# Optimization experiments

Measured on AMD Instinct MI355X. Metric: run time of the kernel, lower is better.

## Reference

```python
import jax, jax.numpy as jnp
import numpy as np

B, V, N, IN_F, HEADS, OUT_F = 4, 4, 1000, 64, 4, 32
D = HEADS * OUT_F  # 128, concat=True
E = 64000
NEG_SLOPE = 0.2


def setup_inputs() -> dict:
    key = jax.random.key(0)
    ks = jax.random.split(key, 8)
    x = jax.random.normal(ks[0], (B, V, N, IN_F), jnp.float32)
    edge_index = jax.random.randint(ks[1], (2, E), 0, B * N, dtype=jnp.int64)
    W = jax.random.normal(ks[2], (HEADS * OUT_F, IN_F), jnp.float32) / np.sqrt(IN_F)
    att = jax.random.normal(ks[3], (1, HEADS, 2 * OUT_F), jnp.float32) * 0.1
    in_proj_w = jax.random.normal(ks[4], (3 * D, D), jnp.float32) / np.sqrt(D)
    in_proj_b = jnp.zeros((3 * D,), jnp.float32)
    out_proj_w = jax.random.normal(ks[5], (D, D), jnp.float32) / np.sqrt(D)
    out_proj_b = jnp.zeros((D,), jnp.float32)
    bias = jnp.zeros((D,), jnp.float32)
    return dict(x=x, W=W, att=att, in_proj_w=in_proj_w, in_proj_b=in_proj_b,
                out_proj_w=out_proj_w, out_proj_b=out_proj_b, bias=bias,
                edge_index=edge_index)


def reference(x, W, att, in_proj_w, in_proj_b, out_proj_w, out_proj_b, bias, edge_index):
    Bx, Vx, Nx, _ = x.shape
    Ntot = Bx * Nx
    # intra-view GAT: shared W across views
    h = jnp.einsum('bvni,oi->bvno', x, W).reshape(Bx, Vx, Nx, HEADS, OUT_F)
    # block-diagonal placement: h_full[b*V+v, b*N:(b+1)*N] = h[b,v]
    ib = jnp.arange(Bx)
    hf = jnp.zeros((Bx, Vx, Bx, Nx, HEADS, OUT_F), x.dtype).at[ib, :, ib].set(h)
    h_full = hf.reshape(Bx * Vx, Ntot, HEADS, OUT_F)
    # add self loops
    loops = jnp.arange(Ntot, dtype=edge_index.dtype)
    src = jnp.concatenate([edge_index[0], loops])
    dst = jnp.concatenate([edge_index[1], loops])
    # attention scores (faithful to source: flatten h_full over (B*V, Ntot) and
    # index with raw node ids, i.e. gathers from block 0 only)
    h_flat = h_full.reshape(Bx * Vx * Ntot, HEADS, OUT_F)
    h_cat = jnp.concatenate([h_flat[src], h_flat[dst]], axis=-1)  # [Etot, H, 2*OUT]
    att_in = jax.nn.leaky_relu(h_cat, NEG_SLOPE)
    scores = jnp.sum(att * att_in, axis=-1)  # [Etot, HEADS]
    # per-destination segment softmax
    seg_max = jax.ops.segment_max(scores, dst, num_segments=Ntot)
    seg_max = jax.lax.stop_gradient(jnp.where(jnp.isfinite(seg_max), seg_max, 0.0))
    ex = jnp.exp(scores - seg_max[dst])
    denom = jax.ops.segment_sum(ex, dst, num_segments=Ntot)
    alpha = ex / (denom[dst] + 1e-16)  # [Etot, HEADS]
    # scatter-add aggregation, broadcast over B*V rows
    msgs = h_full[:, src] * alpha[None, :, :, None]  # [B*V, Etot, H, OUT]
    out_full = jnp.zeros_like(h_full).at[:, dst].add(msgs)
    # extract each graph's own node block
    out = out_full.reshape(Bx, Vx, Bx, Nx, HEADS, OUT_F)[ib, :, ib]  # [B,V,N,H,OUT]
    h_gat = out.reshape(Bx, Vx, Nx, HEADS * OUT_F)  # concat heads
    # inter-view mixing: MHA over the V axis per node
    seq = h_gat.transpose(0, 2, 1, 3).reshape(Bx * Nx, Vx, D)
    q, k, v = jnp.split(seq @ in_proj_w.T + in_proj_b, 3, axis=-1)
    hd = D // HEADS
    sp = lambda t: t.reshape(Bx * Nx, Vx, HEADS, hd).transpose(0, 2, 1, 3)
    q, k, v = sp(q), sp(k), sp(v)
    aw = jax.nn.softmax(jnp.einsum('bhqd,bhkd->bhqk', q, k) / jnp.sqrt(jnp.asarray(hd, x.dtype)), axis=-1)
    ao = jnp.einsum('bhqk,bhkd->bhqd', aw, v).transpose(0, 2, 1, 3).reshape(Bx * Nx, Vx, D)
    mixed = ao @ out_proj_w.T + out_proj_b
    h_mixed = mixed.reshape(Bx, Nx, Vx, D).transpose(0, 2, 1, 3)  # [B,V,N,D]
    return h_mixed + bias
```

## Files before the change

kernel.cpp:

```cpp
#include <hip/hip_runtime.h>

#define NN 1000
#define HEADS_ 4
#define DM 128
#define EE 64000
#define NTOT 4000
#define ETOT 68000
#define CAP 48

template <int K, int SCORE, int REMAP>
__global__ __launch_bounds__(256) void gemm_kernel(const float* __restrict__ A,
                                                   const float* __restrict__ Wt,
                                                   const float* __restrict__ b1,
                                                   const float* __restrict__ b2,
                                                   float* __restrict__ C, int N,
                                                   const float* __restrict__ att,
                                                   float* __restrict__ ssrc,
                                                   float* __restrict__ sdst) {
  __shared__ float As[128 * 64];
  __shared__ float Bs[64 * 64];
  int tid = threadIdx.x;
  int m0 = blockIdx.x * 128, n0 = blockIdx.y * 64;
  int tx = tid & 15, ty = tid >> 4;
  const float4* A4 = (const float4*)A;
  const float4* W4 = (const float4*)Wt;
  float acc[8][4] = {};

  for (int c = 0; c < K / 64; ++c) {
    __syncthreads();
    {
      int q = tid & 15;
      int r0 = tid >> 4;
#pragma unroll
      for (int p = 0; p < 8; ++p) {
        int r = r0 + p * 16;
        float4 v = A4[(size_t)(m0 + r) * (K / 4) + c * 16 + q];
        *(float4*)&As[r * 64 + ((q ^ (r & 15)) << 2)] = v;
      }
#pragma unroll
      for (int p = 0; p < 4; ++p) {
        int r = r0 + p * 16;
        float4 v = W4[(size_t)(n0 + r) * (K / 4) + c * 16 + q];
        *(float4*)&Bs[r * 64 + ((q ^ (r & 15)) << 2)] = v;
      }
    }
    __syncthreads();
#pragma unroll 4
    for (int q = 0; q < 16; ++q) {
      float4 a[8], b[4];
#pragma unroll
      for (int i = 0; i < 8; ++i) {
        int r = ty * 8 + i;
        a[i] = *(const float4*)&As[r * 64 + ((q ^ (r & 15)) << 2)];
      }
#pragma unroll
      for (int j = 0; j < 4; ++j) {
        int rn = tx * 4 + j;
        b[j] = *(const float4*)&Bs[rn * 64 + ((q ^ (rn & 15)) << 2)];
      }
#pragma unroll
      for (int i = 0; i < 8; ++i)
#pragma unroll
        for (int j = 0; j < 4; ++j)
          acc[i][j] += a[i].x * b[j].x + a[i].y * b[j].y
                     + a[i].z * b[j].z + a[i].w * b[j].w;
    }
  }

  float bd[4] = {0.f, 0.f, 0.f, 0.f};
  int nc = n0 + tx * 4;
  if (b1) { bd[0] = b1[nc]; bd[1] = b1[nc+1]; bd[2] = b1[nc+2]; bd[3] = b1[nc+3]; }
  if (b2) { bd[0] += b2[nc]; bd[1] += b2[nc+1]; bd[2] += b2[nc+2]; bd[3] += b2[nc+3]; }
#pragma unroll
  for (int i = 0; i < 8; ++i) {
    int m = m0 + ty * 8 + i;
    int om = m;
    if (REMAP) {
      int node = m >> 2, v = m & 3;
      int b = node / NN, n = node - b * NN;
      om = (b * 4 + v) * NN + n;
    }
    float4 o = make_float4(acc[i][0] + bd[0], acc[i][1] + bd[1],
                           acc[i][2] + bd[2], acc[i][3] + bd[3]);
    *(float4*)&C[(size_t)om * N + nc] = o;
  }

  if (SCORE && m0 < NN) {
    int hsel = tx >> 3;
    int h = (int)blockIdx.y * 2 + hsel;
    int kb = (tx & 7) * 4;
    float a0[4], a1[4];
#pragma unroll
    for (int j = 0; j < 4; ++j) {
      a0[j] = att[h * 64 + kb + j];
      a1[j] = att[h * 64 + 32 + kb + j];
    }
#pragma unroll
    for (int i = 0; i < 8; ++i) {
      int m = m0 + ty * 8 + i;
      float p0 = 0.f, p1 = 0.f;
#pragma unroll
      for (int j = 0; j < 4; ++j) {
        float g = acc[i][j];
        float lr = g > 0.f ? g : 0.2f * g;
        p0 += a0[j] * lr;
        p1 += a1[j] * lr;
      }
      p0 += __shfl_xor(p0, 1, 16); p1 += __shfl_xor(p1, 1, 16);
      p0 += __shfl_xor(p0, 2, 16); p1 += __shfl_xor(p1, 2, 16);
      p0 += __shfl_xor(p0, 4, 16); p1 += __shfl_xor(p1, 4, 16);
      if ((tx & 7) == 0 && m < NN) {
        ssrc[m * HEADS_ + h] = p0;
        sdst[m * HEADS_ + h] = p1;
      }
    }
  }
}

__global__ void edge_score_kernel(const int* __restrict__ ei,
                                  const float* __restrict__ ssrc,
                                  const float* __restrict__ sdst,
                                  float* __restrict__ exbuf,
                                  float* __restrict__ denom,
                                  int* __restrict__ cnt,
                                  int2* __restrict__ elist) {
  int e = blockIdx.x * blockDim.x + threadIdx.x;
  if (e >= ETOT) return;
  int s, d;
  if (e < EE) { s = ei[e]; d = ei[EE + e]; }
  else { s = d = e - EE; }
#pragma unroll
  for (int h = 0; h < HEADS_; ++h) {
    float sc = ssrc[s * HEADS_ + h] + sdst[d * HEADS_ + h];
    float ex = __expf(sc);
    exbuf[e * HEADS_ + h] = ex;
    atomicAdd(&denom[d * HEADS_ + h], ex);
  }
  if (s / NN == d / NN) {
    int pos = atomicAdd(&cnt[d], 1);
    if (pos < CAP) elist[d * CAP + pos] = make_int2(s, e);
  }
}

__global__ __launch_bounds__(256) void gather_kernel(const int* __restrict__ cnt,
                                                     const int2* __restrict__ elist,
                                                     const float* __restrict__ exbuf,
                                                     const float* __restrict__ denom,
                                                     const float* __restrict__ hbuf,
                                                     float* __restrict__ hgat) {
  int li = threadIdx.x >> 7;
  int t = threadIdx.x & 127;
  int d = blockIdx.x * 2 + li;
  int v = t >> 5, q = t & 31;
  int h = q >> 3;
  int b = d / NN;
  float rd = 1.f / (denom[d * HEADS_ + h] + 1e-16f);
  float4 acc = make_float4(0.f, 0.f, 0.f, 0.f);
  int m = cnt[d]; if (m > CAP) m = CAP;
  const int2* el = elist + d * CAP;
  const float* hbase = hbuf + ((size_t)(b * 4 + v) * NN) * DM + q * 4;
  for (int i = 0; i < m; ++i) {
    int2 se = el[i];
    float alpha = exbuf[se.y * HEADS_ + h] * rd;
    int sl = se.x - b * NN;
    float4 hv = *(const float4*)(hbase + (size_t)sl * DM);
    acc.x += alpha * hv.x; acc.y += alpha * hv.y;
    acc.z += alpha * hv.z; acc.w += alpha * hv.w;
  }
  *(float4*)&hgat[((size_t)(d * 4 + v)) * DM + q * 4] = acc;
}

__global__ __launch_bounds__(256) void attn_kernel(const float* __restrict__ qkv,
                                                   float* __restrict__ ao) {
  int li = threadIdx.x >> 7;
  int t = threadIdx.x & 127;
  int node = blockIdx.x * 2 + li;
  __shared__ float qs[2][4][DM], ks[2][4][DM], vs[2][4][DM];
  __shared__ float aw[2][4][HEADS_][4];
#pragma unroll
  for (int v = 0; v < 4; ++v) {
    size_t base = (size_t)(node * 4 + v) * 384;
    qs[li][v][t] = qkv[base + t];
    ks[li][v][t] = qkv[base + 128 + t];
    vs[li][v][t] = qkv[base + 256 + t];
  }
  __syncthreads();
  if (t < 64) {
    int vq = t >> 4, vk = (t >> 2) & 3, h = t & 3;
    float acc = 0.f;
#pragma unroll
    for (int kd = 0; kd < 32; ++kd)
      acc += qs[li][vq][h * 32 + kd] * ks[li][vk][h * 32 + kd];
    aw[li][vq][h][vk] = acc * 0.17677669529663687f;
  }
  __syncthreads();
  if (t < 16) {
    int vq = t >> 2, h = t & 3;
    float m = aw[li][vq][h][0];
    for (int i = 1; i < 4; ++i) m = fmaxf(m, aw[li][vq][h][i]);
    float e[4], s = 0.f;
    for (int i = 0; i < 4; ++i) { e[i] = __expf(aw[li][vq][h][i] - m); s += e[i]; }
    for (int i = 0; i < 4; ++i) aw[li][vq][h][i] = e[i] / s;
  }
  __syncthreads();
  int h = t >> 5;
#pragma unroll
  for (int vq = 0; vq < 4; ++vq) {
    float acc = 0.f;
#pragma unroll
    for (int vk = 0; vk < 4; ++vk) acc += aw[li][vq][h][vk] * vs[li][vk][t];
    ao[(size_t)(node * 4 + vq) * DM + t] = acc;
  }
}

extern "C" void kernel_launch(void* const* d_in, const int* in_sizes, int n_in,
                              void* d_out, int out_size, void* d_ws, size_t ws_size,
                              hipStream_t stream) {
  const float* x    = (const float*)d_in[0];
  const float* W    = (const float*)d_in[1];
  const float* att  = (const float*)d_in[2];
  const float* inw  = (const float*)d_in[3];
  const float* inb  = (const float*)d_in[4];
  const float* outw = (const float*)d_in[5];
  const float* outb = (const float*)d_in[6];
  const float* bias = (const float*)d_in[7];
  const int*   ei   = (const int*)d_in[8];
  float* out = (float*)d_out;

  float* ws = (float*)d_ws;
  float* hbuf  = ws;
  float* hgat  = ws + 2100000;
  float* qkv   = ws + 4200000;
  float* ao    = ws + 10400000;
  float* ssrc  = ws + 12500000;
  float* sdst  = ssrc + 16000;
  float* denom = sdst + 16000;
  int*   cnt   = (int*)(denom + 16000);
  float* exbuf = (float*)(cnt + 4000);
  int2*  elist = (int2*)(exbuf + 272000);

  hipMemsetAsync(ssrc, 0, 52000 * sizeof(float), stream);

  gemm_kernel<64, 1, 0><<<dim3(125, 2), 256, 0, stream>>>(
      x, W, nullptr, nullptr, hbuf, 128, att, ssrc, sdst);
  edge_score_kernel<<<(ETOT + 255) / 256, 256, 0, stream>>>(
      ei, ssrc, sdst, exbuf, denom, cnt, elist);
  gather_kernel<<<NTOT / 2, 256, 0, stream>>>(cnt, elist, exbuf, denom, hbuf, hgat);
  gemm_kernel<128, 0, 0><<<dim3(125, 6), 256, 0, stream>>>(
      hgat, inw, inb, nullptr, qkv, 384, nullptr, nullptr, nullptr);
  attn_kernel<<<NTOT / 2, 256, 0, stream>>>(qkv, ao);
  gemm_kernel<128, 0, 1><<<dim3(125, 2), 256, 0, stream>>>(
      ao, outw, outb, bias, out, 128, nullptr, nullptr, nullptr);
}
```

Before: 171.8 us.

## Fuse all stages into one cooperative persistent kernel with grid syncs

Replaces six separate launches and a memset with a single cooperative kernel of 256 blocks that runs each stage in turn, separated by grid.sync. The edge pass now only builds per-destination source lists, with no per-edge exp buffer and no atomic denominator. The gather stage computes exp scores and the softmax denominator locally in shared memory and keeps only same-graph sources. This removes launch gaps, the float atomics and the exbuf traffic, at the cost of grid-wide barriers and fewer blocks in flight for the GEMM stages, which now run 750 tiles over 256 blocks.

```diff
diff --git a/kernel.cpp b/kernel.cpp
--- a/kernel.cpp
+++ b/kernel.cpp
@@ -1,4 +1,7 @@
 #include <hip/hip_runtime.h>
+#include <hip/hip_cooperative_groups.h>
+
+namespace cg = cooperative_groups;
 
 #define NN 1000
 #define HEADS_ 4
@@ -7,20 +10,25 @@
 #define NTOT 4000
 #define ETOT 68000
 #define CAP 48
+#define GRID 256
+
+union SMem {
+  struct { float As[128 * 64]; float Bs[64 * 64]; } g;
+  struct { float q[2][4][DM], k[2][4][DM], v[2][4][DM];
+           float aw[2][4][HEADS_][4]; } a;
+  struct { int s[2][CAP]; float ex[2][CAP][HEADS_]; } gat;
+};
 
 template <int K, int SCORE, int REMAP>
-__global__ __launch_bounds__(256) void gemm_kernel(const float* __restrict__ A,
-                                                   const float* __restrict__ Wt,
-                                                   const float* __restrict__ b1,
-                                                   const float* __restrict__ b2,
-                                                   float* __restrict__ C, int N,
-                                                   const float* __restrict__ att,
-                                                   float* __restrict__ ssrc,
-                                                   float* __restrict__ sdst) {
-  __shared__ float As[128 * 64];
-  __shared__ float Bs[64 * 64];
-  int tid = threadIdx.x;
-  int m0 = blockIdx.x * 128, n0 = blockIdx.y * 64;
+__device__ void gemm_tile(SMem* sm, int m0, int n0,
+                          const float* __restrict__ A, const float* __restrict__ Wt,
+                          const float* __restrict__ b1, const float* __restrict__ b2,
+                          float* __restrict__ C, int N,
+                          const float* __restrict__ att,
+                          float* __restrict__ ssrc, float* __restrict__ sdst,
+                          int tid, int by) {
+  float* As = sm->g.As;
+  float* Bs = sm->g.Bs;
   int tx = tid & 15, ty = tid >> 4;
   const float4* A4 = (const float4*)A;
   const float4* W4 = (const float4*)Wt;
@@ -87,7 +95,7 @@
 
   if (SCORE && m0 < NN) {
     int hsel = tx >> 3;
-    int h = (int)blockIdx.y * 2 + hsel;
+    int h = by * 2 + hsel;
     int kb = (tx & 7) * 4;
     float a0[4], a1[4];
 #pragma unroll
@@ -117,99 +125,131 @@
   }
 }
 
-__global__ void edge_score_kernel(const int* __restrict__ ei,
-                                  const float* __restrict__ ssrc,
-                                  const float* __restrict__ sdst,
-                                  float* __restrict__ exbuf,
-                                  float* __restrict__ denom,
-                                  int* __restrict__ cnt,
-                                  int2* __restrict__ elist) {
-  int e = blockIdx.x * blockDim.x + threadIdx.x;
-  if (e >= ETOT) return;
-  int s, d;
-  if (e < EE) { s = ei[e]; d = ei[EE + e]; }
-  else { s = d = e - EE; }
-#pragma unroll
-  for (int h = 0; h < HEADS_; ++h) {
-    float sc = ssrc[s * HEADS_ + h] + sdst[d * HEADS_ + h];
-    float ex = __expf(sc);
-    exbuf[e * HEADS_ + h] = ex;
-    atomicAdd(&denom[d * HEADS_ + h], ex);
-  }
-  if (s / NN == d / NN) {
+__global__ __launch_bounds__(256, 2) void fused_kernel(
+    const float* __restrict__ x, const float* __restrict__ W,
+    const float* __restrict__ att,
+    const float* __restrict__ inw, const float* __restrict__ inb,
+    const float* __restrict__ outw, const float* __restrict__ outb,
+    const float* __restrict__ bias, const int* __restrict__ ei,
+    float* __restrict__ out,
+    float* __restrict__ hbuf, float* __restrict__ hgat,
+    float* __restrict__ qkv, float* __restrict__ ao,
+    float* __restrict__ ssrc, float* __restrict__ sdst,
+    int* __restrict__ cnt, int* __restrict__ elist) {
+  cg::grid_group grid = cg::this_grid();
+  __shared__ SMem sm;
+  int bid = blockIdx.x;
+  int tid = threadIdx.x;
+
+  if (bid < 250) {
+    int by = bid & 1;
+    gemm_tile<64, 1, 0>(&sm, (bid >> 1) * 128, by * 64, x, W, nullptr, nullptr,
+                        hbuf, 128, att, ssrc, sdst, tid, by);
+  } else {
+    for (int idx = (bid - 250) * 256 + tid; idx < 28000; idx += 6 * 256) {
+      if (idx < NTOT) cnt[idx] = 0;
+      int z = idx - NTOT;
+      if (z >= 0 && z < 12000) ssrc[4000 + z] = 0.f;
+      int z2 = z - 12000;
+      if (z2 >= 0) sdst[4000 + z2] = 0.f;
+    }
+  }
+  grid.sync();
+
+  for (int e = bid * 256 + tid; e < ETOT; e += GRID * 256) {
+    int s, d;
+    if (e < EE) { s = ei[e]; d = ei[EE + e]; }
+    else { s = d = e - EE; }
     int pos = atomicAdd(&cnt[d], 1);
-    if (pos < CAP) elist[d * CAP + pos] = make_int2(s, e);
-  }
-}
-
-__global__ __launch_bounds__(256) void gather_kernel(const int* __restrict__ cnt,
-                                                     const int2* __restrict__ elist,
-                                                     const float* __restrict__ exbuf,
-                                                     const float* __restrict__ denom,
-                                                     const float* __restrict__ hbuf,
-                                                     float* __restrict__ hgat) {
-  int li = threadIdx.x >> 7;
-  int t = threadIdx.x & 127;
-  int d = blockIdx.x * 2 + li;
-  int v = t >> 5, q = t & 31;
-  int h = q >> 3;
-  int b = d / NN;
-  float rd = 1.f / (denom[d * HEADS_ + h] + 1e-16f);
-  float4 acc = make_float4(0.f, 0.f, 0.f, 0.f);
-  int m = cnt[d]; if (m > CAP) m = CAP;
-  const int2* el = elist + d * CAP;
-  const float* hbase = hbuf + ((size_t)(b * 4 + v) * NN) * DM + q * 4;
-  for (int i = 0; i < m; ++i) {
-    int2 se = el[i];
-    float alpha = exbuf[se.y * HEADS_ + h] * rd;
-    int sl = se.x - b * NN;
-    float4 hv = *(const float4*)(hbase + (size_t)sl * DM);
-    acc.x += alpha * hv.x; acc.y += alpha * hv.y;
-    acc.z += alpha * hv.z; acc.w += alpha * hv.w;
-  }
-  *(float4*)&hgat[((size_t)(d * 4 + v)) * DM + q * 4] = acc;
-}
-
-__global__ __launch_bounds__(256) void attn_kernel(const float* __restrict__ qkv,
-                                                   float* __restrict__ ao) {
-  int li = threadIdx.x >> 7;
-  int t = threadIdx.x & 127;
-  int node = blockIdx.x * 2 + li;
-  __shared__ float qs[2][4][DM], ks[2][4][DM], vs[2][4][DM];
-  __shared__ float aw[2][4][HEADS_][4];
-#pragma unroll
-  for (int v = 0; v < 4; ++v) {
-    size_t base = (size_t)(node * 4 + v) * 384;
-    qs[li][v][t] = qkv[base + t];
-    ks[li][v][t] = qkv[base + 128 + t];
-    vs[li][v][t] = qkv[base + 256 + t];
-  }
-  __syncthreads();
-  if (t < 64) {
-    int vq = t >> 4, vk = (t >> 2) & 3, h = t & 3;
-    float acc = 0.f;
-#pragma unroll
-    for (int kd = 0; kd < 32; ++kd)
-      acc += qs[li][vq][h * 32 + kd] * ks[li][vk][h * 32 + kd];
-    aw[li][vq][h][vk] = acc * 0.17677669529663687f;
-  }
-  __syncthreads();
-  if (t < 16) {
-    int vq = t >> 2, h = t & 3;
-    float m = aw[li][vq][h][0];
-    for (int i = 1; i < 4; ++i) m = fmaxf(m, aw[li][vq][h][i]);
-    float e[4], s = 0.f;
-    for (int i = 0; i < 4; ++i) { e[i] = __expf(aw[li][vq][h][i] - m); s += e[i]; }
-    for (int i = 0; i < 4; ++i) aw[li][vq][h][i] = e[i] / s;
-  }
-  __syncthreads();
-  int h = t >> 5;
-#pragma unroll
-  for (int vq = 0; vq < 4; ++vq) {
-    float acc = 0.f;
-#pragma unroll
-    for (int vk = 0; vk < 4; ++vk) acc += aw[li][vq][h][vk] * vs[li][vk][t];
-    ao[(size_t)(node * 4 + vq) * DM + t] = acc;
+    if (pos < CAP) elist[d * CAP + pos] = s;
+  }
+  grid.sync();
+
+  for (int p = bid; p < NTOT / 2; p += GRID) {
+    int li = tid >> 7, t = tid & 127;
+    int d = p * 2 + li;
+    int b = d / NN;
+    int v = t >> 5, q = t & 31, h = q >> 3;
+    int m = cnt[d]; if (m > CAP) m = CAP;
+    for (int base = 0; base < m; base += 32) {
+      int i = base + (t >> 2);
+      if (i < m) {
+        int s = elist[d * CAP + i];
+        if ((t & 3) == 0) sm.gat.s[li][i] = s;
+        float sc = ssrc[s * HEADS_ + (t & 3)] + sdst[d * HEADS_ + (t & 3)];
+        sm.gat.ex[li][i][t & 3] = __expf(sc);
+      }
+    }
+    __syncthreads();
+    float den = 1e-16f;
+    float4 acc = make_float4(0.f, 0.f, 0.f, 0.f);
+    const float* hbase = hbuf + ((size_t)(b * 4 + v) * NN) * DM + q * 4;
+    for (int i = 0; i < m; ++i) {
+      float ex = sm.gat.ex[li][i][h];
+      den += ex;
+      unsigned sl = (unsigned)(sm.gat.s[li][i] - b * NN);
+      if (sl < NN) {
+        float4 hv = *(const float4*)(hbase + (size_t)sl * DM);
+        acc.x += ex * hv.x; acc.y += ex * hv.y;
+        acc.z += ex * hv.z; acc.w += ex * hv.w;
+      }
+    }
+    float r = 1.f / den;
+    acc.x *= r; acc.y *= r; acc.z *= r; acc.w *= r;
+    *(float4*)&hgat[((size_t)(d * 4 + v)) * DM + q * 4] = acc;
+    __syncthreads();
+  }
+  grid.sync();
+
+  for (int tId = bid; tId < 750; tId += GRID)
+    gemm_tile<128, 0, 0>(&sm, (tId / 6) * 128, (tId % 6) * 64, hgat, inw, inb,
+                         nullptr, qkv, 384, nullptr, nullptr, nullptr, tid, 0);
+  grid.sync();
+
+  for (int p = bid; p < NTOT / 2; p += GRID) {
+    int li = tid >> 7, t = tid & 127;
+    int node = p * 2 + li;
+#pragma unroll
+    for (int v = 0; v < 4; ++v) {
+      size_t base = (size_t)(node * 4 + v) * 384;
+      sm.a.q[li][v][t] = qkv[base + t];
+      sm.a.k[li][v][t] = qkv[base + 128 + t];
+      sm.a.v[li][v][t] = qkv[base + 256 + t];
+    }
+    __syncthreads();
+    if (t < 64) {
+      int vq = t >> 4, vk = (t >> 2) & 3, h = t & 3;
+      float acc = 0.f;
+#pragma unroll
+      for (int kd = 0; kd < 32; ++kd)
+        acc += sm.a.q[li][vq][h * 32 + kd] * sm.a.k[li][vk][h * 32 + kd];
+      sm.a.aw[li][vq][h][vk] = acc * 0.17677669529663687f;
+    }
+    __syncthreads();
+    if (t < 16) {
+      int vq = t >> 2, h = t & 3;
+      float mx = sm.a.aw[li][vq][h][0];
+      for (int i = 1; i < 4; ++i) mx = fmaxf(mx, sm.a.aw[li][vq][h][i]);
+      float e[4], s = 0.f;
+      for (int i = 0; i < 4; ++i) { e[i] = __expf(sm.a.aw[li][vq][h][i] - mx); s += e[i]; }
+      for (int i = 0; i < 4; ++i) sm.a.aw[li][vq][h][i] = e[i] / s;
+    }
+    __syncthreads();
+    int h = t >> 5;
+#pragma unroll
+    for (int vq = 0; vq < 4; ++vq) {
+      float acc = 0.f;
+#pragma unroll
+      for (int vk = 0; vk < 4; ++vk) acc += sm.a.aw[li][vq][h][vk] * sm.a.v[li][vk][t];
+      ao[(size_t)(node * 4 + vq) * DM + t] = acc;
+    }
+    __syncthreads();
+  }
+  grid.sync();
+
+  if (bid < 250) {
+    gemm_tile<128, 0, 1>(&sm, (bid >> 1) * 128, (bid & 1) * 64, ao, outw, outb,
+                         bias, out, 128, nullptr, nullptr, nullptr, tid, 0);
   }
 }
 
@@ -234,21 +274,14 @@
   float* ao    = ws + 10400000;
   float* ssrc  = ws + 12500000;
   float* sdst  = ssrc + 16000;
-  float* denom = sdst + 16000;
-  int*   cnt   = (int*)(denom + 16000);
-  float* exbuf = (float*)(cnt + 4000);
-  int2*  elist = (int2*)(exbuf + 272000);
-
-  hipMemsetAsync(ssrc, 0, 52000 * sizeof(float), stream);
-
-  gemm_kernel<64, 1, 0><<<dim3(125, 2), 256, 0, stream>>>(
-      x, W, nullptr, nullptr, hbuf, 128, att, ssrc, sdst);
-  edge_score_kernel<<<(ETOT + 255) / 256, 256, 0, stream>>>(
-      ei, ssrc, sdst, exbuf, denom, cnt, elist);
-  gather_kernel<<<NTOT / 2, 256, 0, stream>>>(cnt, elist, exbuf, denom, hbuf, hgat);
-  gemm_kernel<128, 0, 0><<<dim3(125, 6), 256, 0, stream>>>(
-      hgat, inw, inb, nullptr, qkv, 384, nullptr, nullptr, nullptr);
-  attn_kernel<<<NTOT / 2, 256, 0, stream>>>(qkv, ao);
-  gemm_kernel<128, 0, 1><<<dim3(125, 2), 256, 0, stream>>>(
-      ao, outw, outb, bias, out, 128, nullptr, nullptr, nullptr);
+  int*   cnt   = (int*)(sdst + 16000);
+  int*   elist = cnt + 4000;
+
+  void* args[] = {(void*)&x, (void*)&W, (void*)&att, (void*)&inw, (void*)&inb,
+                  (void*)&outw, (void*)&outb, (void*)&bias, (void*)&ei,
+                  (void*)&out, (void*)&hbuf, (void*)&hgat, (void*)&qkv,
+                  (void*)&ao, (void*)&ssrc, (void*)&sdst, (void*)&cnt,
+                  (void*)&elist};
+  (void)hipLaunchCooperativeKernel((const void*)fused_kernel, dim3(GRID),
+                                   dim3(256), args, 0, stream);
 }
```

Measured after the change: 373.2 us. 117% more time.

## Fuse edge bucketing into first GEMM and compute softmax inside gather

Applied to the files above, without the earlier changes.

The first projection GEMM and the edge bucketing now run in one launch, with spare blocks filling per-destination source lists. The separate edge-score kernel, its exp buffer and the atomic denominator accumulation are gone; each gather block recomputes the exps for its destination's edges into shared memory and normalises locally. The shared-memory XOR swizzle of the GEMM tiles is also changed. This removes a launch, global atomics and intermediate traffic, at the cost of the softmax denominator depending on the CAP-limited edge list and extra shared memory in the gather kernel.

```diff
diff --git a/kernel.cpp b/kernel.cpp
--- a/kernel.cpp
+++ b/kernel.cpp
@@ -7,20 +7,19 @@
 #define NTOT 4000
 #define ETOT 68000
 #define CAP 48
+#define EB 34
 
 template <int K, int SCORE, int REMAP>
-__global__ __launch_bounds__(256) void gemm_kernel(const float* __restrict__ A,
-                                                   const float* __restrict__ Wt,
-                                                   const float* __restrict__ b1,
-                                                   const float* __restrict__ b2,
-                                                   float* __restrict__ C, int N,
-                                                   const float* __restrict__ att,
-                                                   float* __restrict__ ssrc,
-                                                   float* __restrict__ sdst) {
+__device__ void gemm_tile(int mi, int ni,
+                          const float* __restrict__ A, const float* __restrict__ Wt,
+                          const float* __restrict__ b1, const float* __restrict__ b2,
+                          float* __restrict__ C, int N,
+                          const float* __restrict__ att,
+                          float* __restrict__ ssrc, float* __restrict__ sdst) {
   __shared__ float As[128 * 64];
   __shared__ float Bs[64 * 64];
   int tid = threadIdx.x;
-  int m0 = blockIdx.x * 128, n0 = blockIdx.y * 64;
+  int m0 = mi * 128, n0 = ni * 64;
   int tx = tid & 15, ty = tid >> 4;
   const float4* A4 = (const float4*)A;
   const float4* W4 = (const float4*)Wt;
@@ -35,13 +34,13 @@
       for (int p = 0; p < 8; ++p) {
         int r = r0 + p * 16;
         float4 v = A4[(size_t)(m0 + r) * (K / 4) + c * 16 + q];
-        *(float4*)&As[r * 64 + ((q ^ (r & 15)) << 2)] = v;
+        *(float4*)&As[r * 64 + ((q ^ ((r >> 2) & 15)) << 2)] = v;
       }
 #pragma unroll
       for (int p = 0; p < 4; ++p) {
         int r = r0 + p * 16;
         float4 v = W4[(size_t)(n0 + r) * (K / 4) + c * 16 + q];
-        *(float4*)&Bs[r * 64 + ((q ^ (r & 15)) << 2)] = v;
+        *(float4*)&Bs[r * 64 + ((q ^ ((r >> 2) & 15)) << 2)] = v;
       }
     }
     __syncthreads();
@@ -51,12 +50,12 @@
 #pragma unroll
       for (int i = 0; i < 8; ++i) {
         int r = ty * 8 + i;
-        a[i] = *(const float4*)&As[r * 64 + ((q ^ (r & 15)) << 2)];
+        a[i] = *(const float4*)&As[r * 64 + ((q ^ ((r >> 2) & 15)) << 2)];
       }
 #pragma unroll
       for (int j = 0; j < 4; ++j) {
         int rn = tx * 4 + j;
-        b[j] = *(const float4*)&Bs[rn * 64 + ((q ^ (rn & 15)) << 2)];
+        b[j] = *(const float4*)&Bs[rn * 64 + ((q ^ ((rn >> 2) & 15)) << 2)];
       }
 #pragma unroll
       for (int i = 0; i < 8; ++i)
@@ -87,7 +86,7 @@
 
   if (SCORE && m0 < NN) {
     int hsel = tx >> 3;
-    int h = (int)blockIdx.y * 2 + hsel;
+    int h = ni * 2 + hsel;
     int kb = (tx & 7) * 4;
     float a0[4], a1[4];
 #pragma unroll
@@ -117,57 +116,78 @@
   }
 }
 
-__global__ void edge_score_kernel(const int* __restrict__ ei,
-                                  const float* __restrict__ ssrc,
-                                  const float* __restrict__ sdst,
-                                  float* __restrict__ exbuf,
-                                  float* __restrict__ denom,
-                                  int* __restrict__ cnt,
-                                  int2* __restrict__ elist) {
-  int e = blockIdx.x * blockDim.x + threadIdx.x;
-  if (e >= ETOT) return;
-  int s, d;
-  if (e < EE) { s = ei[e]; d = ei[EE + e]; }
-  else { s = d = e - EE; }
-#pragma unroll
-  for (int h = 0; h < HEADS_; ++h) {
-    float sc = ssrc[s * HEADS_ + h] + sdst[d * HEADS_ + h];
-    float ex = __expf(sc);
-    exbuf[e * HEADS_ + h] = ex;
-    atomicAdd(&denom[d * HEADS_ + h], ex);
-  }
-  if (s / NN == d / NN) {
-    int pos = atomicAdd(&cnt[d], 1);
-    if (pos < CAP) elist[d * CAP + pos] = make_int2(s, e);
+__global__ __launch_bounds__(256) void k1_kernel(const float* __restrict__ x,
+                                                 const float* __restrict__ W,
+                                                 const float* __restrict__ att,
+                                                 float* __restrict__ hbuf,
+                                                 float* __restrict__ ssrc,
+                                                 float* __restrict__ sdst,
+                                                 const int* __restrict__ ei,
+                                                 int* __restrict__ cnt,
+                                                 int* __restrict__ elist) {
+  int bid = blockIdx.x;
+  if (bid < 250) {
+    gemm_tile<64, 1, 0>(bid >> 1, bid & 1, x, W, nullptr, nullptr, hbuf, 128,
+                        att, ssrc, sdst);
+  } else {
+    for (int e = (bid - 250) * 256 + threadIdx.x; e < ETOT; e += EB * 256) {
+      int s, d;
+      if (e < EE) { s = ei[e]; d = ei[EE + e]; }
+      else { s = d = e - EE; }
+      int pos = atomicAdd(&cnt[d], 1);
+      if (pos < CAP) elist[d * CAP + pos] = s;
+    }
   }
 }
 
 __global__ __launch_bounds__(256) void gather_kernel(const int* __restrict__ cnt,
-                                                     const int2* __restrict__ elist,
-                                                     const float* __restrict__ exbuf,
-                                                     const float* __restrict__ denom,
+                                                     const int* __restrict__ elist,
+                                                     const float* __restrict__ ssrc,
+                                                     const float* __restrict__ sdst,
                                                      const float* __restrict__ hbuf,
                                                      float* __restrict__ hgat) {
+  __shared__ int   srcs[2][CAP];
+  __shared__ float exs[2][CAP][HEADS_];
   int li = threadIdx.x >> 7;
   int t = threadIdx.x & 127;
   int d = blockIdx.x * 2 + li;
-  int v = t >> 5, q = t & 31;
-  int h = q >> 3;
   int b = d / NN;
-  float rd = 1.f / (denom[d * HEADS_ + h] + 1e-16f);
+  int v = t >> 5, q = t & 31, h = q >> 3;
+  int m = cnt[d]; if (m > CAP) m = CAP;
+  for (int base = 0; base < m; base += 32) {
+    int i = base + (t >> 2);
+    if (i < m) {
+      int s = elist[d * CAP + i];
+      if ((t & 3) == 0) srcs[li][i] = s;
+      float sc = ssrc[s * HEADS_ + (t & 3)] + sdst[d * HEADS_ + (t & 3)];
+      exs[li][i][t & 3] = __expf(sc);
+    }
+  }
+  __syncthreads();
+  float den = 1e-16f;
   float4 acc = make_float4(0.f, 0.f, 0.f, 0.f);
-  int m = cnt[d]; if (m > CAP) m = CAP;
-  const int2* el = elist + d * CAP;
   const float* hbase = hbuf + ((size_t)(b * 4 + v) * NN) * DM + q * 4;
   for (int i = 0; i < m; ++i) {
-    int2 se = el[i];
-    float alpha = exbuf[se.y * HEADS_ + h] * rd;
-    int sl = se.x - b * NN;
-    float4 hv = *(const float4*)(hbase + (size_t)sl * DM);
-    acc.x += alpha * hv.x; acc.y += alpha * hv.y;
-    acc.z += alpha * hv.z; acc.w += alpha * hv.w;
-  }
+    float ex = exs[li][i][h];
+    den += ex;
+    unsigned sl = (unsigned)(srcs[li][i] - b * NN);
+    if (sl < NN) {
+      float4 hv = *(const float4*)(hbase + (size_t)sl * DM);
+      acc.x += ex * hv.x; acc.y += ex * hv.y;
+      acc.z += ex * hv.z; acc.w += ex * hv.w;
+    }
+  }
+  float r = 1.f / den;
+  acc.x *= r; acc.y *= r; acc.z *= r; acc.w *= r;
   *(float4*)&hgat[((size_t)(d * 4 + v)) * DM + q * 4] = acc;
+}
+
+__global__ __launch_bounds__(256) void qkv_kernel(const float* __restrict__ hgat,
+                                                  const float* __restrict__ inw,
+                                                  const float* __restrict__ inb,
+                                                  float* __restrict__ qkv) {
+  gemm_tile<128, 0, 0>(blockIdx.x, blockIdx.y, hgat, inw, inb, nullptr, qkv,
+                       384, nullptr, nullptr, nullptr);
 }
 
 __global__ __launch_bounds__(256) void attn_kernel(const float* __restrict__ qkv,
@@ -196,10 +216,10 @@
   __syncthreads();
   if (t < 16) {
     int vq = t >> 2, h = t & 3;
-    float m = aw[li][vq][h][0];
-    for (int i = 1; i < 4; ++i) m = fmaxf(m, aw[li][vq][h][i]);
+    float mx = aw[li][vq][h][0];
+    for (int i = 1; i < 4; ++i) mx = fmaxf(mx, aw[li][vq][h][i]);
     float e[4], s = 0.f;
-    for (int i = 0; i < 4; ++i) { e[i] = __expf(aw[li][vq][h][i] - m); s += e[i]; }
+    for (int i = 0; i < 4; ++i) { e[i] = __expf(aw[li][vq][h][i] - mx); s += e[i]; }
     for (int i = 0; i < 4; ++i) aw[li][vq][h][i] = e[i] / s;
   }
   __syncthreads();
@@ -211,6 +231,15 @@
     for (int vk = 0; vk < 4; ++vk) acc += aw[li][vq][h][vk] * vs[li][vk][t];
     ao[(size_t)(node * 4 + vq) * DM + t] = acc;
   }
+}
+
+__global__ __launch_bounds__(256) void outproj_kernel(const float* __restrict__ ao,
+                                                      const float* __restrict__ outw,
+                                                      const float* __restrict__ outb,
+                                                      const float* __restrict__ bias,
+                                                      float* __restrict__ out) {
+  gemm_tile<128, 0, 1>(blockIdx.x, blockIdx.y, ao, outw, outb, bias, out, 128,
+                       nullptr, nullptr, nullptr);
 }
 
 extern "C" void kernel_launch(void* const* d_in, const int* in_sizes, int n_in,
@@ -234,21 +263,14 @@
   float* ao    = ws + 10400000;
   float* ssrc  = ws + 12500000;
   float* sdst  = ssrc + 16000;
-  float* denom = sdst + 16000;
-  int*   cnt   = (int*)(denom + 16000);
-  float* exbuf = (float*)(cnt + 4000);
-  int2*  elist = (int2*)(exbuf + 272000);
-
-  hipMemsetAsync(ssrc, 0, 52000 * sizeof(float), stream);
-
-  gemm_kernel<64, 1, 0><<<dim3(125, 2), 256, 0, stream>>>(
-      x, W, nullptr, nullptr, hbuf, 128, att, ssrc, sdst);
-  edge_score_kernel<<<(ETOT + 255) / 256, 256, 0, stream>>>(
-      ei, ssrc, sdst, exbuf, denom, cnt, elist);
-  gather_kernel<<<NTOT / 2, 256, 0, stream>>>(cnt, elist, exbuf, denom, hbuf, hgat);
-  gemm_kernel<128, 0, 0><<<dim3(125, 6), 256, 0, stream>>>(
-      hgat, inw, inb, nullptr, qkv, 384, nullptr, nullptr, nullptr);
+  int*   cnt   = (int*)(sdst + 16000);
+  int*   elist = cnt + 4000;
+
+  hipMemsetAsync(ssrc, 0, 36000 * sizeof(float), stream);
+
+  k1_kernel<<<250 + EB, 256, 0, stream>>>(x, W, att, hbuf, ssrc, sdst, ei, cnt, elist);
+  gather_kernel<<<NTOT / 2, 256, 0, stream>>>(cnt, elist, ssrc, sdst, hbuf, hgat);
+  qkv_kernel<<<dim3(125, 6), 256, 0, stream>>>(hgat, inw, inb, qkv);
   attn_kernel<<<NTOT / 2, 256, 0, stream>>>(qkv, ao);
-  gemm_kernel<128, 0, 1><<<dim3(125, 2), 256, 0, stream>>>(
-      ao, outw, outb, bias, out, 128, nullptr, nullptr, nullptr);
-}
+  outproj_kernel<<<dim3(125, 2), 256, 0, stream>>>(ao, outw, outb, bias, out);
+}
```

Result: faster. 151.0 us (median of 2 runs) (-12.1%).
